# Optimization experiments

Hardware: AMD Instinct MI355X
Metric: run time of the kernel (lower is better)

The kernel has to match this reference:

```python
import jax, jax.numpy as jnp
import numpy as np

D = 1024
H = 16
HD = D // H  # 64
FF = 4 * D
EPS = 1e-5

def _layernorm(x, g, b):
    mu = jnp.mean(x, axis=-1, keepdims=True)
    var = jnp.mean((x - mu) ** 2, axis=-1, keepdims=True)
    return (x - mu) * jax.lax.rsqrt(var + EPS) * g + b

def _apply_rotary(x, cos, sin):
    # x: [B,H,T,HD]; cos/sin: [T,HD//2] broadcast over B,H
    d = x.shape[-1] // 2
    x1, x2 = x[..., :d], x[..., d:]
    return jnp.concatenate([x1 * cos - x2 * sin, x2 * cos + x1 * sin], axis=-1)

def setup_inputs() -> dict:
    key = jax.random.key(0)
    ks = jax.random.split(key, 12)
    B, T = 4, 2048
    s = 0.02
    return {
        "x": jax.random.normal(ks[0], (B, T, D), jnp.float32),
        "rope_cos": jax.random.uniform(ks[1], (T, HD // 2), jnp.float32),
        "rope_sin": jax.random.uniform(ks[2], (T, HD // 2), jnp.float32),
        "ln1_g": jnp.ones((D,), jnp.float32),
        "ln1_b": jnp.zeros((D,), jnp.float32),
        "Wqkv": jax.random.normal(ks[3], (D, 3 * D), jnp.float32) * s,
        "bqkv": jnp.zeros((3 * D,), jnp.float32),
        "Wo": jax.random.normal(ks[4], (D, D), jnp.float32) * s,
        "bo": jnp.zeros((D,), jnp.float32),
        "ln2_g": jnp.ones((D,), jnp.float32),
        "ln2_b": jnp.zeros((D,), jnp.float32),
        "W1": jax.random.normal(ks[5], (D, FF), jnp.float32) * s,
        "b1": jnp.zeros((FF,), jnp.float32),
        "W2": jax.random.normal(ks[6], (FF, D), jnp.float32) * s,
        "b2": jnp.zeros((D,), jnp.float32),
    }

def reference(x, rope_cos, rope_sin, ln1_g, ln1_b, Wqkv, bqkv, Wo, bo, ln2_g, ln2_b, W1, b1, W2, b2):
    B, T, _ = x.shape
    h = _layernorm(x, ln1_g, ln1_b)
    qkv = (h @ Wqkv + bqkv).reshape(B, T, 3, H, HD)
    qkv = jnp.transpose(qkv, (2, 0, 3, 1, 4))  # [3,B,H,T,HD]
    q, k, v = qkv[0], qkv[1], qkv[2]
    q = _apply_rotary(q, rope_cos, rope_sin)
    k = _apply_rotary(k, rope_cos, rope_sin)
    scale = 1.0 / jnp.sqrt(jnp.float32(HD))
    scores = jnp.einsum('bhqd,bhkd->bhqk', q, k) * scale
    probs = jax.nn.softmax(scores, axis=-1)
    attn = jnp.einsum('bhqk,bhkd->bhqd', probs, v)
    attn = jnp.transpose(attn, (0, 2, 1, 3)).reshape(B, T, D)
    x = x + attn @ Wo + bo
    h2 = _layernorm(x, ln2_g, ln2_b)
    mlp = jax.nn.gelu(h2 @ W1 + b1, approximate=False) @ W2 + b2
    return x + mlp
```

## Files before the change

kernel.cpp:

```cpp
#include <hip/hip_runtime.h>
#include <hip/hip_bf16.h>
#include <math.h>

typedef __bf16 bf16x8 __attribute__((ext_vector_type(8)));
typedef float f32x4 __attribute__((ext_vector_type(4)));
typedef float f32x16 __attribute__((ext_vector_type(16)));
typedef unsigned short u16x8 __attribute__((ext_vector_type(8)));
typedef unsigned short u16x4 __attribute__((ext_vector_type(4)));
typedef unsigned int u32x4 __attribute__((ext_vector_type(4)));

#define DEV __device__ __forceinline__

DEV unsigned short f2bf(float f) { __bf16 h = (__bf16)f; return __builtin_bit_cast(unsigned short, h); }
DEV float bf2f(unsigned short u) { __bf16 h = __builtin_bit_cast(__bf16, u); return (float)h; }
DEV unsigned int pk2(float a, float b) {
  return (unsigned int)f2bf(a) | ((unsigned int)f2bf(b) << 16);
}

DEV void async_cp16(const void* g, void* l) {
  __builtin_amdgcn_global_load_lds((const __attribute__((address_space(1))) void*)g,
                                   (__attribute__((address_space(3))) void*)l, 16, 0, 0);
}

__global__ __launch_bounds__(256) void ln_kernel(const float* __restrict__ in,
    const float* __restrict__ g, const float* __restrict__ b,
    unsigned short* __restrict__ out)
{
  const int row = blockIdx.x;
  const int tid = threadIdx.x;
  const float4 v = ((const float4*)(in + (size_t)row * 1024))[tid];
  float s  = v.x + v.y + v.z + v.w;
  float sq = v.x*v.x + v.y*v.y + v.z*v.z + v.w*v.w;
  for (int m = 1; m < 64; m <<= 1) { s += __shfl_xor(s, m); sq += __shfl_xor(sq, m); }
  __shared__ float red[8];
  const int wave = tid >> 6;
  if ((tid & 63) == 0) { red[wave] = s; red[4 + wave] = sq; }
  __syncthreads();
  s  = red[0] + red[1] + red[2] + red[3];
  sq = red[4] + red[5] + red[6] + red[7];
  const float mu = s * (1.0f / 1024.0f);
  const float var = sq * (1.0f / 1024.0f) - mu * mu;
  const float rs = rsqrtf(var + 1e-5f);
  const float4 gv = ((const float4*)g)[tid];
  const float4 bv = ((const float4*)b)[tid];
  u16x4 o;
  o[0] = f2bf((v.x - mu) * rs * gv.x + bv.x);
  o[1] = f2bf((v.y - mu) * rs * gv.y + bv.y);
  o[2] = f2bf((v.z - mu) * rs * gv.z + bv.z);
  o[3] = f2bf((v.w - mu) * rs * gv.w + bv.w);
  *(u16x4*)(out + (size_t)row * 1024 + tid * 4) = o;
}

__global__ __launch_bounds__(256) void wtrans_kernel(const float* __restrict__ in,
    unsigned short* __restrict__ out, int K, int N)
{
  __shared__ float tile[32][33];
  const int n0 = blockIdx.x * 32, k0 = blockIdx.y * 32;
  const int r = threadIdx.x >> 5, c = threadIdx.x & 31;
  for (int p = 0; p < 4; ++p)
    tile[r + p * 8][c] = in[(size_t)(k0 + r + p * 8) * N + n0 + c];
  __syncthreads();
  for (int p = 0; p < 4; ++p)
    out[(size_t)(n0 + r + p * 8) * K + k0 + c] = f2bf(tile[c][r + p * 8]);
}

enum { EPI_QKV = 0, EPI_ATTNO = 1, EPI_GELU = 2, EPI_FINAL = 3 };

template <int EPI>
__global__ __launch_bounds__(256, 3) void gemm_bt(
    const unsigned short* __restrict__ A,
    const unsigned short* __restrict__ Bt,
    const float* __restrict__ bias,
    const float* __restrict__ resid,
    void* __restrict__ out,
    int M, int N, int K,
    const float* __restrict__ rc, const float* __restrict__ rsn,
    unsigned short* __restrict__ vout)
{
  __shared__ unsigned short lA[8192] __attribute__((aligned(16)));
  __shared__ unsigned short lB[8192] __attribute__((aligned(16)));
  const int tid = threadIdx.x;
  const int lane = tid & 63, wave = tid >> 6;
  const int l15 = lane & 15, quad = lane >> 4;
  const int bm = blockIdx.x * 128, bn = blockIdx.y * 128;
  const int wm = (wave & 1) * 64, wn = (wave >> 1) * 64;

  const unsigned short* ga[4]; const unsigned short* gb[4];
  unsigned short* la_dst[4]; unsigned short* lb_dst[4];
  for (int it = 0; it < 4; ++it) {
    const int s = it * 256 + tid;
    const int row = s >> 3;
    const int ch = (s & 7) ^ (row & 7);
    ga[it] = A  + (size_t)(bm + row) * K + ch * 8;
    gb[it] = Bt + (size_t)(bn + row) * K + ch * 8;
    const int base = (it * 256 + wave * 64) * 8;
    la_dst[it] = lA + base;
    lb_dst[it] = lB + base;
  }
  int offA[2][4], offB[2][4];
  for (int ks = 0; ks < 2; ++ks)
    for (int i = 0; i < 4; ++i) {
      int row = wm + i * 16 + l15;
      offA[ks][i] = (row * 8 + ((ks * 4 + quad) ^ (row & 7))) * 8;
      row = wn + i * 16 + l15;
      offB[ks][i] = (row * 8 + ((ks * 4 + quad) ^ (row & 7))) * 8;
    }

  f32x4 acc[4][4];
  for (int i = 0; i < 4; ++i)
    for (int j = 0; j < 4; ++j)
      acc[i][j] = f32x4{0.f, 0.f, 0.f, 0.f};

  for (int k0 = 0; k0 < K; k0 += 64) {
    for (int it = 0; it < 4; ++it) async_cp16(ga[it], la_dst[it]);
    for (int it = 0; it < 4; ++it) async_cp16(gb[it], lb_dst[it]);
    for (int it = 0; it < 4; ++it) { ga[it] += 64; gb[it] += 64; }
    __syncthreads();
    for (int ks = 0; ks < 2; ++ks) {
      bf16x8 af[4], bfr[4];
      for (int i = 0; i < 4; ++i) af[i]  = *(const bf16x8*)(lA + offA[ks][i]);
      for (int j = 0; j < 4; ++j) bfr[j] = *(const bf16x8*)(lB + offB[ks][j]);
      for (int i = 0; i < 4; ++i)
        for (int j = 0; j < 4; ++j)
          acc[i][j] = __builtin_amdgcn_mfma_f32_16x16x32_bf16(af[i], bfr[j], acc[i][j], 0, 0, 0);
    }
    __syncthreads();
  }

  float bvals[4];
  for (int j = 0; j < 4; ++j) bvals[j] = bias[bn + wn + j * 16 + l15];

  if constexpr (EPI == EPI_QKV) {
    const int cn = bn + wn;
    const int sec = cn >> 10;
    if (sec == 2) {
      const int b = bm >> 11;
      const int hh = (cn & 1023) >> 6;
      for (int i = 0; i < 4; ++i) {
        const int t0 = (bm + wm + i * 16 + quad * 4) & 2047;
        for (int j = 0; j < 4; ++j) {
          const int d = j * 16 + l15;
          u16x4 o;
          for (int r = 0; r < 4; ++r) o[r] = f2bf(acc[i][j][r] + bvals[j]);
          *(u16x4*)(vout + ((size_t)((b * 16 + hh) * 64 + d)) * 2048 + t0) = o;
        }
      }
    } else {
      const float qscale = (sec == 0) ? 0.18033688f : 1.0f;
      unsigned short* qkvout = (unsigned short*)out;
      for (int i = 0; i < 4; ++i) {
        for (int r = 0; r < 4; ++r) {
          const int row = bm + wm + i * 16 + quad * 4 + r;
          const int t = row & 2047;
          for (int j = 0; j < 2; ++j) {
            const int d = j * 16 + l15;
            const float v1 = acc[i][j][r] + bvals[j];
            const float v2 = acc[i][j + 2][r] + bvals[j + 2];
            const float c = rc[t * 32 + d], s = rsn[t * 32 + d];
            const float o1 = (v1 * c - v2 * s) * qscale;
            const float o2 = (v2 * c + v1 * s) * qscale;
            const size_t base = (size_t)row * 3072 + cn + d;
            qkvout[base] = f2bf(o1);
            qkvout[base + 32] = f2bf(o2);
          }
        }
      }
    }
  } else {
    for (int i = 0; i < 4; ++i) {
      for (int r = 0; r < 4; ++r) {
        const size_t row = bm + wm + i * 16 + quad * 4 + r;
        for (int j = 0; j < 4; ++j) {
          const size_t col = bn + wn + j * 16 + l15;
          const float v = acc[i][j][r] + bvals[j];
          const size_t idx = row * (size_t)N + col;
          if constexpr (EPI == EPI_ATTNO) {
            ((float*)out)[idx] = resid[idx] + v;
          } else if constexpr (EPI == EPI_GELU) {
            const float gl = 0.5f * v * (1.0f + erff(v * 0.70710678118f));
            ((unsigned short*)out)[idx] = f2bf(gl);
          } else {
            ((float*)out)[idx] = resid[idx] + v;
          }
        }
      }
    }
  }
}

__global__ __launch_bounds__(256, 4) void attn_kernel(
    const unsigned short* __restrict__ qkv,
    const unsigned short* __restrict__ vt,
    unsigned short* __restrict__ outb)
{
  __shared__ unsigned short Ks[2][4096] __attribute__((aligned(16)));
  __shared__ unsigned short Vs[2][4096] __attribute__((aligned(16)));
  __shared__ float Sred[128];

  const int tid = threadIdx.x;
  const int lane = tid & 63, wave = tid >> 6;
  const int l31 = lane & 31, hl = lane >> 5;
  const int bh = blockIdx.y, b = bh >> 4, h = bh & 15;
  const int q0 = blockIdx.x * 128;
  const int qsub = wave * 32;

  bf16x8 qf[4];
  {
    const unsigned short* qp = qkv + (size_t)(b * 2048 + q0 + qsub + l31) * 3072 + h * 64 + hl * 8;
    for (int kc = 0; kc < 4; ++kc) qf[kc] = *(const bf16x8*)(qp + kc * 16);
  }

  const int s0 = wave * 128 + lane, s1 = s0 + 64;
  const int r0 = s0 >> 3, c0 = (lane & 7) ^ (r0 & 7);
  const int r1 = s1 >> 3, c1 = (lane & 7) ^ (r1 & 7);
  const unsigned short* kbase = qkv + (size_t)(b * 2048) * 3072 + 1024 + h * 64;
  const unsigned short* ks0 = kbase + (size_t)r0 * 3072 + c0 * 8;
  const unsigned short* ks1 = kbase + (size_t)r1 * 3072 + c1 * 8;
  const unsigned short* vbase = vt + (size_t)bh * 64 * 2048;
  const unsigned short* vs0 = vbase + (size_t)r0 * 2048 + c0 * 8;
  const unsigned short* vs1 = vbase + (size_t)r1 * 2048 + c1 * 8;
  unsigned short* kd[2] = { Ks[0] + wave * 1024, Ks[1] + wave * 1024 };
  unsigned short* vd[2] = { Vs[0] + wave * 1024, Vs[1] + wave * 1024 };

  int offK[2][4], offV[2][4];
  for (int g = 0; g < 2; ++g)
    for (int kc = 0; kc < 4; ++kc) {
      const int rk = g * 32 + l31;
      offK[g][kc] = (rk * 8 + ((2 * kc + hl) ^ (rk & 7))) * 8;
    }
  for (int dn = 0; dn < 2; ++dn)
    for (int t = 0; t < 4; ++t) {
      const int rv = dn * 32 + l31;
      offV[dn][t] = (rv * 8 + ((2 * t + hl) ^ (rv & 7))) * 8;
    }

  f32x16 accO[2];
  for (int dn = 0; dn < 2; ++dn)
    for (int i = 0; i < 16; ++i) accO[dn][i] = 0.f;
  float rsum = 0.f;

  async_cp16(ks0, kd[0]);
  async_cp16(ks1, kd[0] + 512);
  async_cp16(vs0, vd[0]);
  async_cp16(vs1, vd[0] + 512);

  for (int kt = 0; kt < 32; ++kt) {
    const int cur = kt & 1, nxt = cur ^ 1;
    __syncthreads();
    if (kt < 31) {
      const size_t ko = (size_t)(kt + 1) * 64 * 3072;
      const int vo = (kt + 1) * 64;
      async_cp16(ks0 + ko, kd[nxt]);
      async_cp16(ks1 + ko, kd[nxt] + 512);
      async_cp16(vs0 + vo, vd[nxt]);
      async_cp16(vs1 + vo, vd[nxt] + 512);
    }
    for (int g = 0; g < 2; ++g) {
      f32x16 accS;
      for (int i = 0; i < 16; ++i) accS[i] = 0.f;
      for (int kc = 0; kc < 4; ++kc) {
        const bf16x8 kf = *(const bf16x8*)(Ks[cur] + offK[g][kc]);
        accS = __builtin_amdgcn_mfma_f32_32x32x16_bf16(kf, qf[kc], accS, 0, 0, 0);
      }
      float p[16];
      for (int i = 0; i < 16; ++i) {
        p[i] = __builtin_amdgcn_exp2f(accS[i]);
        rsum += p[i];
      }
      for (int c = 0; c < 2; ++c) {
        const unsigned int xlo0 = pk2(p[8 * c + 0], p[8 * c + 1]);
        const unsigned int xlo1 = pk2(p[8 * c + 2], p[8 * c + 3]);
        const unsigned int xhi0 = pk2(p[8 * c + 4], p[8 * c + 5]);
        const unsigned int xhi1 = pk2(p[8 * c + 6], p[8 * c + 7]);
        const unsigned int recv0 = __shfl_xor((int)(hl ? xlo0 : xhi0), 32);
        const unsigned int recv1 = __shfl_xor((int)(hl ? xlo1 : xhi1), 32);
        u32x4 w;
        w[0] = hl ? recv0 : xlo0;
        w[1] = hl ? recv1 : xlo1;
        w[2] = hl ? xhi0 : recv0;
        w[3] = hl ? xhi1 : recv1;
        const bf16x8 pf = __builtin_bit_cast(bf16x8, w);
        const int t = 2 * g + c;
        for (int dn = 0; dn < 2; ++dn) {
          const bf16x8 vf = *(const bf16x8*)(Vs[cur] + offV[dn][t]);
          accO[dn] = __builtin_amdgcn_mfma_f32_32x32x16_bf16(pf, vf, accO[dn], 0, 0, 0);
        }
      }
    }
  }

  {
    const float rs2 = rsum + __shfl_xor(rsum, 32);
    if (hl == 0) Sred[qsub + l31] = rs2;
  }
  __syncthreads();
  for (int reg = 0; reg < 16; ++reg) {
    const int rq = qsub + (reg & 3) + 8 * (reg >> 2) + 4 * hl;
    const float inv = 1.0f / Sred[rq];
    const size_t row = (size_t)(b * 2048 + q0 + rq);
    for (int dn = 0; dn < 2; ++dn)
      outb[row * 1024 + h * 64 + dn * 32 + l31] = f2bf(accO[dn][reg] * inv);
  }
}

extern "C" void kernel_launch(void* const* d_in, const int* in_sizes, int n_in,
                              void* d_out, int out_size, void* d_ws, size_t ws_size,
                              hipStream_t stream)
{
  const float* x        = (const float*)d_in[0];
  const float* rope_cos = (const float*)d_in[1];
  const float* rope_sin = (const float*)d_in[2];
  const float* ln1_g    = (const float*)d_in[3];
  const float* ln1_b    = (const float*)d_in[4];
  const float* Wqkv     = (const float*)d_in[5];
  const float* bqkv     = (const float*)d_in[6];
  const float* Wo       = (const float*)d_in[7];
  const float* bo       = (const float*)d_in[8];
  const float* ln2_g    = (const float*)d_in[9];
  const float* ln2_b    = (const float*)d_in[10];
  const float* W1       = (const float*)d_in[11];
  const float* b1       = (const float*)d_in[12];
  const float* W2       = (const float*)d_in[13];
  const float* b2       = (const float*)d_in[14];
  float* outp = (float*)d_out;

  char* ws = (char*)d_ws;
  size_t off = 0;
  auto alloc = [&](size_t bytes) -> void* {
    void* p = ws + off;
    off += (bytes + 255) & ~(size_t)255;
    return p;
  };
  unsigned short* h1    = (unsigned short*)alloc(8192ull * 1024 * 2);
  unsigned short* wqkvT = (unsigned short*)alloc(3072ull * 1024 * 2);
  unsigned short* woT   = (unsigned short*)alloc(1024ull * 1024 * 2);
  unsigned short* w1T   = (unsigned short*)alloc(4096ull * 1024 * 2);
  unsigned short* w2T   = (unsigned short*)alloc(1024ull * 4096 * 2);
  unsigned short* qkv   = (unsigned short*)alloc(8192ull * 3072 * 2);
  unsigned short* vtb   = (unsigned short*)alloc(64ull * 64 * 2048 * 2);
  unsigned short* h2    = (unsigned short*)alloc(8192ull * 1024 * 2);
  unsigned short* ffb   = (unsigned short*)alloc(8192ull * 4096 * 2);

  wtrans_kernel<<<dim3(96, 32), 256, 0, stream>>>(Wqkv, wqkvT, 1024, 3072);
  wtrans_kernel<<<dim3(32, 32), 256, 0, stream>>>(Wo, woT, 1024, 1024);
  wtrans_kernel<<<dim3(128, 32), 256, 0, stream>>>(W1, w1T, 1024, 4096);
  wtrans_kernel<<<dim3(32, 128), 256, 0, stream>>>(W2, w2T, 4096, 1024);

  ln_kernel<<<8192, 256, 0, stream>>>(x, ln1_g, ln1_b, h1);
  gemm_bt<EPI_QKV><<<dim3(64, 24), 256, 0, stream>>>(h1, wqkvT, bqkv, nullptr, qkv,
                                                     8192, 3072, 1024, rope_cos, rope_sin, vtb);
  attn_kernel<<<dim3(16, 64), 256, 0, stream>>>(qkv, vtb, h1);
  gemm_bt<EPI_ATTNO><<<dim3(64, 8), 256, 0, stream>>>(h1, woT, bo, x, d_out,
                                                      8192, 1024, 1024, nullptr, nullptr, nullptr);
  ln_kernel<<<8192, 256, 0, stream>>>(outp, ln2_g, ln2_b, h2);
  gemm_bt<EPI_GELU><<<dim3(64, 32), 256, 0, stream>>>(h2, w1T, b1, nullptr, ffb,
                                                      8192, 4096, 1024, nullptr, nullptr, nullptr);
  gemm_bt<EPI_FINAL><<<dim3(64, 8), 256, 0, stream>>>(ffb, w2T, b2, outp, d_out,
                                                      8192, 1024, 4096, nullptr, nullptr, nullptr);
}
```

Before: 508.6 us.

## Add 256x256 eight-wave GEMM with phased prefetch for QKV and MLP-up

```diff
diff --git a/kernel.cpp b/kernel.cpp
--- a/kernel.cpp
+++ b/kernel.cpp
@@ -21,6 +21,10 @@
   __builtin_amdgcn_global_load_lds((const __attribute__((address_space(1))) void*)g,
                                    (__attribute__((address_space(3))) void*)l, 16, 0, 0);
 }
+
+#define PHASE_BAR()  do { __builtin_amdgcn_s_barrier(); __builtin_amdgcn_sched_barrier(0); } while (0)
+#define WAIT_LGKM0() do { asm volatile("s_waitcnt lgkmcnt(0)" ::: "memory"); __builtin_amdgcn_sched_barrier(0); } while (0)
+#define WAIT_VM(n)   do { asm volatile("s_waitcnt vmcnt(" #n ")" ::: "memory"); __builtin_amdgcn_sched_barrier(0); } while (0)
 
 __global__ __launch_bounds__(256) void ln_kernel(const float* __restrict__ in,
     const float* __restrict__ g, const float* __restrict__ b,
@@ -130,13 +134,146 @@
   float bvals[4];
   for (int j = 0; j < 4; ++j) bvals[j] = bias[bn + wn + j * 16 + l15];
 
+  for (int i = 0; i < 4; ++i) {
+    for (int r = 0; r < 4; ++r) {
+      const size_t row = bm + wm + i * 16 + quad * 4 + r;
+      for (int j = 0; j < 4; ++j) {
+        const size_t col = bn + wn + j * 16 + l15;
+        const float v = acc[i][j][r] + bvals[j];
+        const size_t idx = row * (size_t)N + col;
+        if constexpr (EPI == EPI_ATTNO) {
+          ((float*)out)[idx] = resid[idx] + v;
+        } else if constexpr (EPI == EPI_GELU) {
+          const float gl = 0.5f * v * (1.0f + erff(v * 0.70710678118f));
+          ((unsigned short*)out)[idx] = f2bf(gl);
+        } else {
+          ((float*)out)[idx] = resid[idx] + v;
+        }
+      }
+    }
+  }
+}
+
+template <int EPI>
+__global__ __launch_bounds__(512, 2) void gemm256(
+    const unsigned short* __restrict__ A,
+    const unsigned short* __restrict__ Bt,
+    const float* __restrict__ bias,
+    void* __restrict__ out,
+    int M, int N, int K,
+    const float* __restrict__ rc, const float* __restrict__ rsn,
+    unsigned short* __restrict__ vout)
+{
+  __shared__ unsigned short lA[2][16384] __attribute__((aligned(16)));
+  __shared__ unsigned short lB[2][16384] __attribute__((aligned(16)));
+  const int tid = threadIdx.x;
+  const int lane = tid & 63, wave = tid >> 6;
+  const int l15 = lane & 15, quad = lane >> 4;
+  const int bm = blockIdx.x * 256, bn = blockIdx.y * 256;
+  const int wr = wave >> 2, wc = wave & 3;
+  const int wm = wr * 128, wn = wc * 64;
+
+  const unsigned short* gA[4]; const unsigned short* gB[4];
+  {
+    const int r0 = tid >> 3;
+    const int ch = (tid & 7) ^ (r0 & 7);
+    for (int it = 0; it < 4; ++it) {
+      gA[it] = A  + (size_t)(bm + it * 64 + r0) * K + ch * 8;
+      gB[it] = Bt + (size_t)(bn + it * 64 + r0) * K + ch * 8;
+    }
+  }
+  const int ldsbase = wave * 512;
+
+  const int swz = l15 & 7;
+  const int oA0 = (wm + l15) * 64 + ((quad) ^ swz) * 8;
+  const int oA1 = (wm + l15) * 64 + ((4 + quad) ^ swz) * 8;
+  const int oB0 = (wn + l15) * 64 + ((quad) ^ swz) * 8;
+  const int oB1 = (wn + l15) * 64 + ((4 + quad) ^ swz) * 8;
+
+  f32x4 acc[8][4];
+  for (int i = 0; i < 8; ++i)
+    for (int j = 0; j < 4; ++j)
+      acc[i][j] = f32x4{0.f, 0.f, 0.f, 0.f};
+
+  const int NT = K >> 6;
+
+  async_cp16(gB[0], lB[0] + 0    + ldsbase);
+  async_cp16(gB[1], lB[0] + 4096 + ldsbase);
+  async_cp16(gB[2], lB[0] + 8192 + ldsbase);
+  async_cp16(gB[3], lB[0] + 12288 + ldsbase);
+  async_cp16(gA[0], lA[0] + 0    + ldsbase);
+  async_cp16(gA[2], lA[0] + 8192 + ldsbase);
+  async_cp16(gA[1], lA[0] + 4096 + ldsbase);
+  async_cp16(gA[3], lA[0] + 12288 + ldsbase);
+  for (int it = 0; it < 4; ++it) { gA[it] += 64; gB[it] += 64; }
+  WAIT_VM(2);
+  PHASE_BAR();
+
+  for (int t = 0; t < NT; ++t) {
+    const unsigned short* lAc = lA[t & 1];
+    const unsigned short* lBc = lB[t & 1];
+    unsigned short* lAn = lA[(t & 1) ^ 1];
+    unsigned short* lBn = lB[(t & 1) ^ 1];
+    const bool pf = (t + 1 < NT);
+    bf16x8 af[4], bfr[4];
+
+    for (int i = 0; i < 4; ++i) af[i]  = *(const bf16x8*)(lAc + oA0 + i * 1024);
+    for (int j = 0; j < 4; ++j) bfr[j] = *(const bf16x8*)(lBc + oB0 + j * 1024);
+    if (pf) { async_cp16(gB[0], lBn + 0 + ldsbase); async_cp16(gB[1], lBn + 4096 + ldsbase); }
+    PHASE_BAR(); WAIT_LGKM0();
+    __builtin_amdgcn_s_setprio(1);
+    for (int i = 0; i < 4; ++i)
+      for (int j = 0; j < 4; ++j)
+        acc[i][j] = __builtin_amdgcn_mfma_f32_16x16x32_bf16(af[i], bfr[j], acc[i][j], 0, 0, 0);
+    __builtin_amdgcn_s_setprio(0);
+    if (pf) { WAIT_VM(2); } else { WAIT_VM(0); }
+    PHASE_BAR();
+
+    for (int i = 0; i < 4; ++i) af[i] = *(const bf16x8*)(lAc + oA0 + (4 + i) * 1024);
+    if (pf) { async_cp16(gB[2], lBn + 8192 + ldsbase); async_cp16(gB[3], lBn + 12288 + ldsbase); }
+    PHASE_BAR(); WAIT_LGKM0();
+    __builtin_amdgcn_s_setprio(1);
+    for (int i = 0; i < 4; ++i)
+      for (int j = 0; j < 4; ++j)
+        acc[4 + i][j] = __builtin_amdgcn_mfma_f32_16x16x32_bf16(af[i], bfr[j], acc[4 + i][j], 0, 0, 0);
+    __builtin_amdgcn_s_setprio(0);
+    PHASE_BAR();
+
+    for (int i = 0; i < 4; ++i) af[i]  = *(const bf16x8*)(lAc + oA1 + i * 1024);
+    for (int j = 0; j < 4; ++j) bfr[j] = *(const bf16x8*)(lBc + oB1 + j * 1024);
+    if (pf) { async_cp16(gA[0], lAn + 0 + ldsbase); async_cp16(gA[2], lAn + 8192 + ldsbase); }
+    PHASE_BAR(); WAIT_LGKM0();
+    __builtin_amdgcn_s_setprio(1);
+    for (int i = 0; i < 4; ++i)
+      for (int j = 0; j < 4; ++j)
+        acc[i][j] = __builtin_amdgcn_mfma_f32_16x16x32_bf16(af[i], bfr[j], acc[i][j], 0, 0, 0);
+    __builtin_amdgcn_s_setprio(0);
+    PHASE_BAR();
+
+    for (int i = 0; i < 4; ++i) af[i] = *(const bf16x8*)(lAc + oA1 + (4 + i) * 1024);
+    if (pf) { async_cp16(gA[1], lAn + 4096 + ldsbase); async_cp16(gA[3], lAn + 12288 + ldsbase); }
+    PHASE_BAR(); WAIT_LGKM0();
+    __builtin_amdgcn_s_setprio(1);
+    for (int i = 0; i < 4; ++i)
+      for (int j = 0; j < 4; ++j)
+        acc[4 + i][j] = __builtin_amdgcn_mfma_f32_16x16x32_bf16(af[i], bfr[j], acc[4 + i][j], 0, 0, 0);
+    __builtin_amdgcn_s_setprio(0);
+    if (pf) { WAIT_VM(2); }
+    PHASE_BAR();
+
+    if (pf) for (int it = 0; it < 4; ++it) { gA[it] += 64; gB[it] += 64; }
+  }
+
+  float bvals[4];
+  for (int j = 0; j < 4; ++j) bvals[j] = bias[bn + wn + j * 16 + l15];
+
   if constexpr (EPI == EPI_QKV) {
     const int cn = bn + wn;
     const int sec = cn >> 10;
     if (sec == 2) {
       const int b = bm >> 11;
       const int hh = (cn & 1023) >> 6;
-      for (int i = 0; i < 4; ++i) {
+      for (int i = 0; i < 8; ++i) {
         const int t0 = (bm + wm + i * 16 + quad * 4) & 2047;
         for (int j = 0; j < 4; ++j) {
           const int d = j * 16 + l15;
@@ -148,15 +285,15 @@
     } else {
       const float qscale = (sec == 0) ? 0.18033688f : 1.0f;
       unsigned short* qkvout = (unsigned short*)out;
-      for (int i = 0; i < 4; ++i) {
+      for (int i = 0; i < 8; ++i) {
         for (int r = 0; r < 4; ++r) {
           const int row = bm + wm + i * 16 + quad * 4 + r;
-          const int t = row & 2047;
+          const int tt = row & 2047;
           for (int j = 0; j < 2; ++j) {
             const int d = j * 16 + l15;
             const float v1 = acc[i][j][r] + bvals[j];
             const float v2 = acc[i][j + 2][r] + bvals[j + 2];
-            const float c = rc[t * 32 + d], s = rsn[t * 32 + d];
+            const float c = rc[tt * 32 + d], s = rsn[tt * 32 + d];
             const float o1 = (v1 * c - v2 * s) * qscale;
             const float o2 = (v2 * c + v1 * s) * qscale;
             const size_t base = (size_t)row * 3072 + cn + d;
@@ -167,24 +304,17 @@
       }
     }
   } else {
-    for (int i = 0; i < 4; ++i) {
+    unsigned short* o = (unsigned short*)out;
+    for (int i = 0; i < 8; ++i)
       for (int r = 0; r < 4; ++r) {
         const size_t row = bm + wm + i * 16 + quad * 4 + r;
         for (int j = 0; j < 4; ++j) {
           const size_t col = bn + wn + j * 16 + l15;
           const float v = acc[i][j][r] + bvals[j];
-          const size_t idx = row * (size_t)N + col;
-          if constexpr (EPI == EPI_ATTNO) {
-            ((float*)out)[idx] = resid[idx] + v;
-          } else if constexpr (EPI == EPI_GELU) {
-            const float gl = 0.5f * v * (1.0f + erff(v * 0.70710678118f));
-            ((unsigned short*)out)[idx] = f2bf(gl);
-          } else {
-            ((float*)out)[idx] = resid[idx] + v;
-          }
+          const float gl = 0.5f * v * (1.0f + erff(v * 0.70710678118f));
+          o[row * (size_t)N + col] = f2bf(gl);
         }
       }
-    }
   }
 }
 
@@ -272,13 +402,13 @@
         const unsigned int xlo1 = pk2(p[8 * c + 2], p[8 * c + 3]);
         const unsigned int xhi0 = pk2(p[8 * c + 4], p[8 * c + 5]);
         const unsigned int xhi1 = pk2(p[8 * c + 6], p[8 * c + 7]);
-        const unsigned int recv0 = __shfl_xor((int)(hl ? xlo0 : xhi0), 32);
-        const unsigned int recv1 = __shfl_xor((int)(hl ? xlo1 : xhi1), 32);
+        const auto sw0 = __builtin_amdgcn_permlane32_swap(xlo0, xhi0, false, false);
+        const auto sw1 = __builtin_amdgcn_permlane32_swap(xlo1, xhi1, false, false);
         u32x4 w;
-        w[0] = hl ? recv0 : xlo0;
-        w[1] = hl ? recv1 : xlo1;
-        w[2] = hl ? xhi0 : recv0;
-        w[3] = hl ? xhi1 : recv1;
+        w[0] = sw0[0];
+        w[1] = sw1[0];
+        w[2] = sw0[1];
+        w[3] = sw1[1];
         const bf16x8 pf = __builtin_bit_cast(bf16x8, w);
         const int t = 2 * g + c;
         for (int dn = 0; dn < 2; ++dn) {
@@ -347,13 +477,13 @@
   wtrans_kernel<<<dim3(32, 128), 256, 0, stream>>>(W2, w2T, 4096, 1024);
 
   ln_kernel<<<8192, 256, 0, stream>>>(x, ln1_g, ln1_b, h1);
-  gemm_bt<EPI_QKV><<<dim3(64, 24), 256, 0, stream>>>(h1, wqkvT, bqkv, nullptr, qkv,
+  gemm256<EPI_QKV><<<dim3(32, 12), 512, 0, stream>>>(h1, wqkvT, bqkv, qkv,
                                                      8192, 3072, 1024, rope_cos, rope_sin, vtb);
   attn_kernel<<<dim3(16, 64), 256, 0, stream>>>(qkv, vtb, h1);
   gemm_bt<EPI_ATTNO><<<dim3(64, 8), 256, 0, stream>>>(h1, woT, bo, x, d_out,
                                                       8192, 1024, 1024, nullptr, nullptr, nullptr);
   ln_kernel<<<8192, 256, 0, stream>>>(outp, ln2_g, ln2_b, h2);
-  gemm_bt<EPI_GELU><<<dim3(64, 32), 256, 0, stream>>>(h2, w1T, b1, nullptr, ffb,
+  gemm256<EPI_GELU><<<dim3(32, 16), 512, 0, stream>>>(h2, w1T, b1, ffb,
                                                       8192, 4096, 1024, nullptr, nullptr, nullptr);
   gemm_bt<EPI_FINAL><<<dim3(64, 8), 256, 0, stream>>>(ffb, w2T, b2, outp, d_out,
                                                       8192, 1024, 4096, nullptr, nullptr, nullptr);
```

Result: slower. 598.3 us (+17.6%).
